# Kernel tuning notes

Measured on AMD Instinct MI355X. Metric: run time of the kernel, lower is better.

Reference implementation:

```python
import jax, jax.numpy as jnp
import numpy as np

L, H, T, C, OUT, B = 8, 16, 2048, 1024, 1024, 4
DH = C // H
EPS = 1e-5


def _sincos_pos_embed(embed_dim, n):
    omega = np.arange(embed_dim // 2, dtype=np.float64) / (embed_dim / 2.0)
    omega = 1.0 / 10000 ** omega
    out = np.einsum('m,d->md', np.arange(n, dtype=np.float64), omega)
    return np.concatenate([np.sin(out), np.cos(out)], axis=1).astype(np.float32)


def setup_inputs() -> dict:
    key = jax.random.key(0)
    ks = jax.random.split(key, 12)
    s = 0.02  # torch init std
    n = lambda k, sh: jax.random.normal(k, sh, jnp.float32) * s
    zc = jnp.zeros((L, C), jnp.float32)
    return {
        'seq': jax.random.normal(ks[0], (B, T, C), jnp.float32),
        'pos_embed': jnp.asarray(_sincos_pos_embed(C, T))[None],  # [1,T,C]
        'Wq': n(ks[1], (L, C, C)), 'bq': zc,
        'Wk': n(ks[2], (L, C, C)), 'bk': zc,
        'Wv': n(ks[3], (L, C, C)), 'bv': zc,
        'Wo': n(ks[4], (L, C, C)), 'bo': zc,
        'ln1_w': jnp.ones((L, C), jnp.float32), 'ln1_b': zc,
        'ln2_w': jnp.ones((L, C), jnp.float32), 'ln2_b': zc,
        'W1': n(ks[5], (L, 4 * C, C)), 'b1': jnp.zeros((L, 4 * C), jnp.float32),
        'W2': n(ks[6], (L, C, 4 * C)), 'b2': zc,
        'lnf_w': jnp.ones((C,), jnp.float32), 'lnf_b': jnp.zeros((C,), jnp.float32),
        'Whead': n(ks[7], (OUT, C)),
    }


def _ln(x, w, b):
    mu = jnp.mean(x, -1, keepdims=True)
    var = jnp.mean(jnp.square(x - mu), -1, keepdims=True)
    return (x - mu) * jax.lax.rsqrt(var + EPS) * w + b


def _block(x, p):
    (Wq, bq, Wk, bk, Wv, bv, Wo, bo, l1w, l1b, l2w, l2b, W1, b1, W2, b2) = p
    b_, t_, c_ = x.shape
    h = _ln(x, l1w, l1b)
    q = (h @ Wq.T + bq).reshape(b_, t_, H, DH)
    k = (h @ Wk.T + bk).reshape(b_, t_, H, DH)
    v = (h @ Wv.T + bv).reshape(b_, t_, H, DH)
    # NOTE: source mask buffer is all ones -> no masking (full softmax)
    att = jnp.einsum('bqhd,bkhd->bhqk', q, k) * (1.0 / np.sqrt(DH))
    att = jax.nn.softmax(att, axis=-1)
    y = jnp.einsum('bhqk,bkhd->bqhd', att, v).reshape(b_, t_, c_)
    x = x + y @ Wo.T + bo
    h2 = _ln(x, l2w, l2b)
    x = x + jax.nn.gelu(h2 @ W1.T + b1, approximate=False) @ W2.T + b2
    return x, None


def reference(seq, pos_embed, Wq, bq, Wk, bk, Wv, bv, Wo, bo,
              ln1_w, ln1_b, ln2_w, ln2_b, W1, b1, W2, b2,
              lnf_w, lnf_b, Whead):
    t = seq.shape[1]
    x = seq + pos_embed[:, -t:, :]  # embedding dropout is identity at eval
    params = (Wq, bq, Wk, bk, Wv, bv, Wo, bo, ln1_w, ln1_b, ln2_w, ln2_b, W1, b1, W2, b2)
    x, _ = jax.lax.scan(_block, x, params)
    x = _ln(x, lnf_w, lnf_b)
    return x @ Whead.T
```

## Files before the change

kernel.cpp:

```cpp
#include <hip/hip_runtime.h>
#include <hip/hip_bf16.h>


#define LAYERS 8
#define NH 16
#define TT 2048
#define CC 1024
#define NB 4
#define MR (NB*TT)
#define LN_EPS 1e-5f

typedef __bf16 bf16_t;
typedef __attribute__((ext_vector_type(8))) __bf16 bf16x8;
typedef __attribute__((ext_vector_type(4))) __bf16 bf16x4;
typedef __attribute__((ext_vector_type(4))) float f32x4;
typedef __attribute__((ext_vector_type(8))) short s16x8;
typedef __attribute__((ext_vector_type(4))) unsigned u32x4;

__device__ inline f32x4 mfma16x16x32(bf16x8 a, bf16x8 b, f32x4 c) {
    return __builtin_amdgcn_mfma_f32_16x16x32_bf16(a, b, c, 0, 0, 0);
}

__device__ inline void gload_lds16(const void* g, void* lds) {
    __builtin_amdgcn_global_load_lds((const __attribute__((address_space(1))) void*)g,
                                     (__attribute__((address_space(3))) void*)lds, 16, 0, 0);
}

__device__ inline unsigned pack_bf16(float a, float b) {
    unsigned short ua = __builtin_bit_cast(unsigned short, (bf16_t)a);
    unsigned short ub = __builtin_bit_cast(unsigned short, (bf16_t)b);
    return (unsigned)ua | ((unsigned)ub << 16);
}


__global__ __launch_bounds__(256) void add_pos_k(const float* __restrict__ s,
                                                 const float* __restrict__ p,
                                                 float* __restrict__ x) {
    int i = blockIdx.x * 256 + threadIdx.x;
    float4 a = ((const float4*)s)[i];
    float4 b = ((const float4*)p)[i & ((TT * CC / 4) - 1)];
    ((float4*)x)[i] = make_float4(a.x + b.x, a.y + b.y, a.z + b.z, a.w + b.w);
}

__global__ __launch_bounds__(256) void f32_to_bf16_k(const float* __restrict__ s,
                                                     bf16_t* __restrict__ d, int n4) {
    int i = blockIdx.x * 256 + threadIdx.x;
    if (i < n4) {
        float4 v = ((const float4*)s)[i];
        bf16x4 o;
        o[0] = (bf16_t)v.x; o[1] = (bf16_t)v.y; o[2] = (bf16_t)v.z; o[3] = (bf16_t)v.w;
        ((bf16x4*)d)[i] = o;
    }
}

__global__ __launch_bounds__(256) void convert_layer_k(
        const float* __restrict__ Wq, const float* __restrict__ Wk,
        const float* __restrict__ Wv, const float* __restrict__ Wo,
        const float* __restrict__ W1, const float* __restrict__ W2,
        const float* __restrict__ bq, const float* __restrict__ bk,
        const float* __restrict__ bv,
        bf16_t* __restrict__ wqkvb, bf16_t* __restrict__ wob,
        bf16_t* __restrict__ w1b, bf16_t* __restrict__ w2b,
        float* __restrict__ bqkv) {
    const int i = blockIdx.x * 256 + threadIdx.x;
    if (i < 3145728) {
        const float4* s4;
        bf16_t* dst;
        int off;
        if (i < 262144)       { s4 = (const float4*)Wq + i;             dst = wqkvb; off = i; }
        else if (i < 524288)  { s4 = (const float4*)Wk + (i - 262144);  dst = wqkvb; off = i; }
        else if (i < 786432)  { s4 = (const float4*)Wv + (i - 524288);  dst = wqkvb; off = i; }
        else if (i < 1048576) { s4 = (const float4*)Wo + (i - 786432);  dst = wob;   off = i - 786432; }
        else if (i < 2097152) { s4 = (const float4*)W1 + (i - 1048576); dst = w1b;   off = i - 1048576; }
        else                  { s4 = (const float4*)W2 + (i - 2097152); dst = w2b;   off = i - 2097152; }
        float4 v = *s4;
        bf16x4 o;
        o[0] = (bf16_t)v.x; o[1] = (bf16_t)v.y; o[2] = (bf16_t)v.z; o[3] = (bf16_t)v.w;
        ((bf16x4*)dst)[off] = o;
    } else if (i < 3146496) {
        const int j = i - 3145728;
        const float* b = (j < 256) ? bq : (j < 512 ? bk : bv);
        ((float4*)bqkv)[j] = ((const float4*)b)[j & 255];
    }
}


__global__ __launch_bounds__(256) void ln_rows_k(const float* __restrict__ x,
                                                 const float* __restrict__ wgt,
                                                 const float* __restrict__ bgt,
                                                 bf16_t* __restrict__ out) {
    const int row = blockIdx.x * 4 + (threadIdx.x >> 6);
    const int l = threadIdx.x & 63;
    const float* xr = x + (size_t)row * CC;
    float4 v[4];
    float s = 0.f, sq = 0.f;
#pragma unroll
    for (int j = 0; j < 4; j++) {
        v[j] = *(const float4*)&xr[j * 256 + l * 4];
        s  += v[j].x + v[j].y + v[j].z + v[j].w;
        sq += v[j].x * v[j].x + v[j].y * v[j].y + v[j].z * v[j].z + v[j].w * v[j].w;
    }
#pragma unroll
    for (int m = 1; m < 64; m <<= 1) { s += __shfl_xor(s, m); sq += __shfl_xor(sq, m); }
    const float mu = s * (1.f / CC);
    const float rstd = rsqrtf(sq * (1.f / CC) - mu * mu + LN_EPS);
#pragma unroll
    for (int j = 0; j < 4; j++) {
        const int c0 = j * 256 + l * 4;
        const float4 wv = *(const float4*)&wgt[c0];
        const float4 bv = *(const float4*)&bgt[c0];
        bf16x4 o;
        o[0] = (bf16_t)((v[j].x - mu) * rstd * wv.x + bv.x);
        o[1] = (bf16_t)((v[j].y - mu) * rstd * wv.y + bv.y);
        o[2] = (bf16_t)((v[j].z - mu) * rstd * wv.z + bv.z);
        o[3] = (bf16_t)((v[j].w - mu) * rstd * wv.w + bv.w);
        *(bf16x4*)&out[(size_t)row * CC + c0] = o;
    }
}


#define EPI_BF16 0
#define EPI_GELU 1
#define EPI_RES  2
#define EPI_F32  3

template <int EPI>
__global__ __launch_bounds__(256) void gemm_bt(const bf16_t* __restrict__ A,
                                               const bf16_t* __restrict__ Bw,
                                               const float* __restrict__ bias,
                                               float* __restrict__ resid,
                                               bf16_t* __restrict__ obf,
                                               float* __restrict__ of32,
                                               int N, int K, int nbn) {
    __shared__ __align__(16) bf16_t As[128 * 32];
    __shared__ __align__(16) bf16_t Bs[128 * 32];
    const int nwg = gridDim.x;
    const int id = blockIdx.x;
    const int swz = (id & 7) * (nwg >> 3) + (id >> 3);
    const int bn = swz % nbn, bm = swz / nbn;
    const int t = threadIdx.x, w = t >> 6, l = t & 63;
    const int wm = (w >> 1) << 6, wn = (w & 1) << 6;
    const int fr = l & 15, fg = l >> 4;
    const int srow = l >> 2, scol = (l & 3) * 8;
    f32x4 acc[4][4] = {};
    for (int k0 = 0; k0 < K; k0 += 32) {
#pragma unroll
        for (int it = 0; it < 2; ++it) {
            const int rr = it * 64 + w * 16;
            gload_lds16(A  + (size_t)(bm * 128 + rr + srow) * K + k0 + scol, &As[rr * 32]);
            gload_lds16(Bw + (size_t)(bn * 128 + rr + srow) * K + k0 + scol, &Bs[rr * 32]);
        }
        __syncthreads();
        bf16x8 af[4], bfv[4];
#pragma unroll
        for (int i = 0; i < 4; i++) af[i]  = *(const bf16x8*)&As[(wm + i * 16 + fr) * 32 + fg * 8];
#pragma unroll
        for (int j = 0; j < 4; j++) bfv[j] = *(const bf16x8*)&Bs[(wn + j * 16 + fr) * 32 + fg * 8];
#pragma unroll
        for (int i = 0; i < 4; i++)
#pragma unroll
            for (int j = 0; j < 4; j++)
                acc[i][j] = mfma16x16x32(af[i], bfv[j], acc[i][j]);
        __syncthreads();
    }
#pragma unroll
    for (int i = 0; i < 4; i++) {
#pragma unroll
        for (int j = 0; j < 4; j++) {
            const int col = bn * 128 + wn + j * 16 + fr;
            float bv = 0.f;
            if constexpr (EPI != EPI_F32) bv = bias[col];
#pragma unroll
            for (int rg = 0; rg < 4; ++rg) {
                const int row = bm * 128 + wm + i * 16 + fg * 4 + rg;
                float v = acc[i][j][rg] + bv;
                if constexpr (EPI == EPI_BF16) {
                    obf[(size_t)row * N + col] = (bf16_t)v;
                } else if constexpr (EPI == EPI_GELU) {
                    v = 0.5f * v * (1.0f + erff(v * 0.70710678118f));
                    obf[(size_t)row * N + col] = (bf16_t)v;
                } else if constexpr (EPI == EPI_RES) {
                    resid[(size_t)row * CC + col] += v;
                } else {
                    of32[(size_t)row * N + col] = v;
                }
            }
        }
    }
}


template <int EPI>
__global__ __launch_bounds__(512, 1) void gemm8p(const bf16_t* __restrict__ A,
                                                 const bf16_t* __restrict__ Bw,
                                                 const float* __restrict__ bias,
                                                 bf16_t* __restrict__ obf,
                                                 int N, int K, int nbn) {
    extern __shared__ __align__(16) char smem[];
    bf16_t* ldsA = (bf16_t*)smem;
    bf16_t* ldsB = (bf16_t*)smem + 24576;
    const int nwg = gridDim.x;
    const int id  = blockIdx.x;
    const int swzid = (id & 7) * (nwg >> 3) + (id >> 3);
    const int bn = swzid % nbn, bm = swzid / nbn;
    const int t = threadIdx.x, wv = t >> 6, lane = t & 63;
    const int fr = lane & 15, fg = lane >> 4;
    const int wm2 = (wv >> 2) * 128, wn2 = (wv & 3) * 64;
    const int swf = ((fr & 8) ? 16 : 0) | ((fr & 4) ? 8 : 0);
    const int rdA0 = (wm2 + fr) * 32 + ((fg * 8) ^ swf);
    const int rdB0 = (wn2 + fr) * 32 + ((fg * 8) ^ swf);
    const int rr0 = wv * 16 + (lane >> 2);
    const int sws = ((rr0 & 8) ? 16 : 0) | ((rr0 & 4) ? 8 : 0);
    const size_t gA0 = (size_t)(bm * 256 + rr0) * K + (((lane & 3) * 8) ^ sws);
    const size_t gB0 = (size_t)(bn * 256 + rr0) * K + (((lane & 3) * 8) ^ sws);
    const int ldsStage = wv * 512;
    const int NT = K >> 5;

    f32x4 acc[8][4] = {};

    auto stA = [&](int T) {
        bf16_t* dst = ldsA + (T % 3) * 8192 + ldsStage;
        const bf16_t* s = A + gA0 + (size_t)T * 32;
        gload_lds16(s, dst);
        gload_lds16(s + (size_t)128 * K, dst + 4096);
    };
    auto stB = [&](int T) {
        bf16_t* dst = ldsB + (T % 3) * 8192 + ldsStage;
        const bf16_t* s = Bw + gB0 + (size_t)T * 32;
        gload_lds16(s, dst);
        gload_lds16(s + (size_t)128 * K, dst + 4096);
    };
    stA(0); stB(0); stA(1); stB(1);

    for (int T = 0; T < NT; ++T) {
        if (T == NT - 1) asm volatile("s_waitcnt vmcnt(0)" ::: "memory");
        else             asm volatile("s_waitcnt vmcnt(4)" ::: "memory");
        __builtin_amdgcn_s_barrier();
        const bf16_t* As_ = ldsA + (T % 3) * 8192;
        const bf16_t* Bs_ = ldsB + (T % 3) * 8192;
        bf16x8 af[4], bf[4];
#pragma unroll
        for (int i = 0; i < 4; i++) af[i] = *(const bf16x8*)&As_[rdA0 + i * 512];
#pragma unroll
        for (int i = 0; i < 4; i++) bf[i] = *(const bf16x8*)&Bs_[rdB0 + i * 512];
        if (T + 2 < NT) stA(T + 2);
        __builtin_amdgcn_s_setprio(1);
#pragma unroll
        for (int mi = 0; mi < 4; mi++)
#pragma unroll
            for (int ni = 0; ni < 4; ni++)
                acc[mi][ni] = mfma16x16x32(af[mi], bf[ni], acc[mi][ni]);
        __builtin_amdgcn_s_setprio(0);
#pragma unroll
        for (int i = 0; i < 4; i++) af[i] = *(const bf16x8*)&As_[rdA0 + (4 + i) * 512];
        if (T + 2 < NT) stB(T + 2);
        __builtin_amdgcn_s_setprio(1);
#pragma unroll
        for (int mi = 0; mi < 4; mi++)
#pragma unroll
            for (int ni = 0; ni < 4; ni++)
                acc[4 + mi][ni] = mfma16x16x32(af[mi], bf[ni], acc[4 + mi][ni]);
        __builtin_amdgcn_s_setprio(0);
    }
#pragma unroll
    for (int mi = 0; mi < 8; mi++) {
#pragma unroll
        for (int ni = 0; ni < 4; ni++) {
            const int col = bn * 256 + wn2 + ni * 16 + fr;
            const float bv = bias[col];
#pragma unroll
            for (int rg = 0; rg < 4; rg++) {
                const int row = bm * 256 + wm2 + mi * 16 + fg * 4 + rg;
                float v = acc[mi][ni][rg] + bv;
                if constexpr (EPI == EPI_GELU)
                    v = 0.5f * v * (1.0f + erff(v * 0.70710678118f));
                obf[(size_t)row * N + col] = (bf16_t)v;
            }
        }
    }
}


__global__ __launch_bounds__(256, 4) void attn_k(const bf16_t* __restrict__ qkv,
                                                 bf16_t* __restrict__ y) {
    __shared__ __align__(16) bf16_t Ks[64 * 64];
    __shared__ __align__(16) bf16_t Vt[64 * 64];
    const int id = blockIdx.x;
    const int swz = (id & 7) * 256 + (id >> 3);
    const int qt = swz & 31, bh = swz >> 5;
    const int b = bh >> 4, h = bh & 15;
    const int t = threadIdx.x, w = t >> 6, l = t & 63;
    const int fr = l & 15, fg = l >> 4;
    const int hh = fg >> 1;
    const int q0 = qt * 64 + w * 16;
    const size_t bT = (size_t)b * TT;
    const float SCL = 0.125f * 1.44269504f;

    bf16x8 qf[2];
    {
        const size_t qoff = (bT + q0 + fr) * 3072 + h * 64 + fg * 8;
        qf[0] = *(const bf16x8*)&qkv[qoff];
        qf[1] = *(const bf16x8*)&qkv[qoff + 32];
    }
    float mrun = -1e30f, lse = 0.f;
    f32x4 oacc[4] = {};

    const int srow = t >> 2;
    const int c8a = (t & 3) * 8;
    const int ksw = (srow & 7) << 4;
    char* KsB = (char*)Ks;
    char* VtB = (char*)Vt;

    s16x8 kr0, kr1, vr0, vr1;
    auto preload = [&](int kv0) {
        const size_t roff = (bT + kv0 + srow) * 3072 + h * 64;
        kr0 = *(const s16x8*)&qkv[roff + 1024 + c8a];
        kr1 = *(const s16x8*)&qkv[roff + 1024 + c8a + 32];
        vr0 = *(const s16x8*)&qkv[roff + 2048 + c8a];
        vr1 = *(const s16x8*)&qkv[roff + 2048 + c8a + 32];
    };
    preload(0);

    for (int kv0 = 0; kv0 < TT; kv0 += 64) {
        __syncthreads();
#pragma unroll
        for (int half = 0; half < 2; ++half) {
            const s16x8 kr = half ? kr1 : kr0;
            const s16x8 vr = half ? vr1 : vr0;
            const int c8 = c8a + half * 32;
            *(s16x8*)(KsB + srow * 128 + ((c8 * 2) ^ ksw)) = kr;
#pragma unroll
            for (int j = 0; j < 8; j++) {
                const int d = c8 + j;
                const int dsw = (((d & 7) ^ ((d >> 3) & 7)) << 4);
                *(short*)(VtB + d * 128 + ((srow * 2) ^ dsw)) = vr[j];
            }
        }
        __syncthreads();
        if (kv0 + 64 < TT) preload(kv0 + 64);

        f32x4 sacc[4] = {};
#pragma unroll
        for (int nt = 0; nt < 4; nt++) {
            const int kr_ = nt * 16 + fr;
            const int sw = (kr_ & 7) << 4;
#pragma unroll
            for (int c = 0; c < 2; c++) {
                bf16x8 kf = *(const bf16x8*)(KsB + kr_ * 128 + ((c * 64 + fg * 16) ^ sw));
                sacc[nt] = mfma16x16x32(kf, qf[c], sacc[nt]);
            }
        }
        float tm = sacc[0][0];
#pragma unroll
        for (int nt = 0; nt < 4; nt++)
#pragma unroll
            for (int rg = 0; rg < 4; rg++) tm = fmaxf(tm, sacc[nt][rg]);
        tm = fmaxf(tm, __shfl_xor(tm, 16));
        tm = fmaxf(tm, __shfl_xor(tm, 32));
        tm *= SCL;
        if (!__all(tm - mrun <= 11.5f)) {
            const float mn = fmaxf(mrun, tm);
            const float co = exp2f(mrun - mn);
            lse *= co; mrun = mn;
            const float cr0 = __shfl(co, fg * 4 + 0);
            const float cr1 = __shfl(co, fg * 4 + 1);
            const float cr2 = __shfl(co, fg * 4 + 2);
            const float cr3 = __shfl(co, fg * 4 + 3);
#pragma unroll
            for (int nd = 0; nd < 4; nd++) {
                oacc[nd][0] *= cr0; oacc[nd][1] *= cr1;
                oacc[nd][2] *= cr2; oacc[nd][3] *= cr3;
            }
        }
        const f32x4 sA0 = hh ? sacc[1] : sacc[0];
        const f32x4 sA1 = hh ? sacc[3] : sacc[2];
        const f32x4 sB0 = hh ? sacc[0] : sacc[1];
        const f32x4 sB1 = hh ? sacc[2] : sacc[3];
        float rs = 0.f;
        unsigned pkA[4], pkB[4];
#pragma unroll
        for (int rg = 0; rg < 4; rg++) {
            const float a0 = exp2f(sA0[rg] * SCL - mrun);
            const float a1 = exp2f(sA1[rg] * SCL - mrun);
            const float b0 = exp2f(sB0[rg] * SCL - mrun);
            const float b1 = exp2f(sB1[rg] * SCL - mrun);
            rs += (a0 + a1) + (b0 + b1);
            pkA[rg] = pack_bf16(a0, a1);
            pkB[rg] = pack_bf16(b0, b1);
        }
        rs += __shfl_xor(rs, 16);
        rs += __shfl_xor(rs, 32);
        lse += rs;
        unsigned s0pk[4], s1pk[4];
#pragma unroll
        for (int rg = 0; rg < 4; rg++) {
            const unsigned r16 = __shfl_xor(pkA[rg], 16);
            const unsigned r32 = __shfl_xor(pkB[rg], 32);
            const unsigned r48 = __shfl_xor(pkB[rg], 48);
            s0pk[rg] = (fg == 0) ? pkA[rg] : (fg == 1) ? r48 : (fg == 2) ? r32 : r16;
            s1pk[rg] = (fg == 0) ? r16 : (fg == 1) ? r32 : (fg == 2) ? r48 : pkA[rg];
        }
        u32x4 w0v, w1v;
        w0v[0] = (s0pk[0] & 0xFFFFu) | (s0pk[1] << 16);
        w0v[1] = (s0pk[2] & 0xFFFFu) | (s0pk[3] << 16);
        w0v[2] = (s1pk[0] & 0xFFFFu) | (s1pk[1] << 16);
        w0v[3] = (s1pk[2] & 0xFFFFu) | (s1pk[3] << 16);
        w1v[0] = (s0pk[0] >> 16) | (s0pk[1] & 0xFFFF0000u);
        w1v[1] = (s0pk[2] >> 16) | (s0pk[3] & 0xFFFF0000u);
        w1v[2] = (s1pk[0] >> 16) | (s1pk[1] & 0xFFFF0000u);
        w1v[3] = (s1pk[2] >> 16) | (s1pk[3] & 0xFFFF0000u);
        const bf16x8 paf0 = __builtin_bit_cast(bf16x8, w0v);
        const bf16x8 paf1 = __builtin_bit_cast(bf16x8, w1v);
#pragma unroll
        for (int nd = 0; nd < 4; nd++) {
            const int dr = nd * 16 + fr;
            const int dsw = (((dr & 7) ^ ((dr >> 3) & 7)) << 4);
            bf16x8 vf0 = *(const bf16x8*)(VtB + dr * 128 + ((fg * 16) ^ dsw));
            oacc[nd] = mfma16x16x32(paf0, vf0, oacc[nd]);
            bf16x8 vf1 = *(const bf16x8*)(VtB + dr * 128 + ((64 + fg * 16) ^ dsw));
            oacc[nd] = mfma16x16x32(paf1, vf1, oacc[nd]);
        }
    }
    const float inv = 1.f / lse;
    const float i0 = __shfl(inv, fg * 4 + 0);
    const float i1 = __shfl(inv, fg * 4 + 1);
    const float i2 = __shfl(inv, fg * 4 + 2);
    const float i3 = __shfl(inv, fg * 4 + 3);
#pragma unroll
    for (int nd = 0; nd < 4; nd++) {
        const size_t ro = (bT + q0 + fg * 4) * CC + h * 64 + nd * 16 + fr;
        y[ro]          = (bf16_t)(oacc[nd][0] * i0);
        y[ro + CC]     = (bf16_t)(oacc[nd][1] * i1);
        y[ro + 2 * CC] = (bf16_t)(oacc[nd][2] * i2);
        y[ro + 3 * CC] = (bf16_t)(oacc[nd][3] * i3);
    }
}


extern "C" void kernel_launch(void* const* d_in, const int* in_sizes, int n_in,
                              void* d_out, int out_size, void* d_ws, size_t ws_size,
                              hipStream_t stream) {
    (void)in_sizes; (void)n_in; (void)out_size; (void)ws_size;
    const float* seq  = (const float*)d_in[0];
    const float* pos  = (const float*)d_in[1];
    const float* Wq   = (const float*)d_in[2];
    const float* bq   = (const float*)d_in[3];
    const float* Wk   = (const float*)d_in[4];
    const float* bk   = (const float*)d_in[5];
    const float* Wv   = (const float*)d_in[6];
    const float* bv   = (const float*)d_in[7];
    const float* Wo   = (const float*)d_in[8];
    const float* bo   = (const float*)d_in[9];
    const float* ln1w = (const float*)d_in[10];
    const float* ln1b = (const float*)d_in[11];
    const float* ln2w = (const float*)d_in[12];
    const float* ln2b = (const float*)d_in[13];
    const float* W1   = (const float*)d_in[14];
    const float* b1   = (const float*)d_in[15];
    const float* W2   = (const float*)d_in[16];
    const float* b2   = (const float*)d_in[17];
    const float* lnfw = (const float*)d_in[18];
    const float* lnfb = (const float*)d_in[19];
    const float* Wh   = (const float*)d_in[20];
    float* out = (float*)d_out;

    char* ws = (char*)d_ws;
    float*  x     = (float*)(ws + 0);
    bf16_t* qkvb  = (bf16_t*)(ws + 33554432);
    bf16_t* yb    = (bf16_t*)(ws + 83886080);
    bf16_t* a1b   = (bf16_t*)(ws + 33554432);
    bf16_t* hb    = (bf16_t*)(ws + 100663296);
    bf16_t* wqkvb = (bf16_t*)(ws + 117440512);
    bf16_t* wob   = (bf16_t*)(ws + 123731968);
    bf16_t* w1b   = (bf16_t*)(ws + 125829120);
    bf16_t* w2b   = (bf16_t*)(ws + 134217728);
    bf16_t* whb   = (bf16_t*)(ws + 142606336);
    float*  bqkv  = (float*)(ws + 144703488);

    hipFuncSetAttribute(reinterpret_cast<const void*>(gemm8p<EPI_BF16>),
                        hipFuncAttributeMaxDynamicSharedMemorySize, 98304);
    hipFuncSetAttribute(reinterpret_cast<const void*>(gemm8p<EPI_GELU>),
                        hipFuncAttributeMaxDynamicSharedMemorySize, 98304);

    f32_to_bf16_k<<<1024, 256, 0, stream>>>(Wh, whb, 262144);
    add_pos_k<<<8192, 256, 0, stream>>>(seq, pos, x);

    for (int l = 0; l < LAYERS; ++l) {
        const size_t wo_ = (size_t)l * CC * CC;
        const size_t w4_ = (size_t)l * 4 * CC * CC;
        convert_layer_k<<<12291, 256, 0, stream>>>(Wq + wo_, Wk + wo_, Wv + wo_, Wo + wo_,
                                                   W1 + w4_, W2 + w4_,
                                                   bq + l * CC, bk + l * CC, bv + l * CC,
                                                   wqkvb, wob, w1b, w2b, bqkv);

        ln_rows_k<<<2048, 256, 0, stream>>>(x, ln1w + l * CC, ln1b + l * CC, hb);
        gemm8p<EPI_BF16><<<384, 512, 98304, stream>>>(hb, wqkvb, bqkv, qkvb,
                                                      3072, 1024, 12);
        attn_k<<<2048, 256, 0, stream>>>(qkvb, yb);
        gemm_bt<EPI_RES><<<512, 256, 0, stream>>>(yb, wob, bo + l * CC, x,
                                                  nullptr, nullptr, 1024, 1024, 8);
        ln_rows_k<<<2048, 256, 0, stream>>>(x, ln2w + l * CC, ln2b + l * CC, hb);
        gemm8p<EPI_GELU><<<512, 512, 98304, stream>>>(hb, w1b, b1 + (size_t)l * 4 * CC,
                                                      a1b, 4096, 1024, 16);
        gemm_bt<EPI_RES><<<512, 256, 0, stream>>>(a1b, w2b, b2 + l * CC, x,
                                                  nullptr, nullptr, 1024, 4096, 8);
    }
    ln_rows_k<<<2048, 256, 0, stream>>>(x, lnfw, lnfb, hb);
    gemm_bt<EPI_F32><<<512, 256, 0, stream>>>(hb, whb, nullptr, nullptr,
                                              nullptr, out, 1024, 1024, 8);
}
```

Baseline: 4.310 ms.

## Process two 16-row query groups per wave in attention to reuse K/V tiles

```diff
diff --git a/kernel.cpp b/kernel.cpp
--- a/kernel.cpp
+++ b/kernel.cpp
@@ -286,24 +286,26 @@
     __shared__ __align__(16) bf16_t Ks[64 * 64];
     __shared__ __align__(16) bf16_t Vt[64 * 64];
     const int id = blockIdx.x;
-    const int swz = (id & 7) * 256 + (id >> 3);
-    const int qt = swz & 31, bh = swz >> 5;
+    const int swz = (id & 7) * 128 + (id >> 3);
+    const int qt = swz & 15, bh = swz >> 4;
     const int b = bh >> 4, h = bh & 15;
     const int t = threadIdx.x, w = t >> 6, l = t & 63;
     const int fr = l & 15, fg = l >> 4;
     const int hh = fg >> 1;
-    const int q0 = qt * 64 + w * 16;
+    const int q0w = qt * 128 + w * 32;
     const size_t bT = (size_t)b * TT;
     const float SCL = 0.125f * 1.44269504f;
 
-    bf16x8 qf[2];
-    {
-        const size_t qoff = (bT + q0 + fr) * 3072 + h * 64 + fg * 8;
-        qf[0] = *(const bf16x8*)&qkv[qoff];
-        qf[1] = *(const bf16x8*)&qkv[qoff + 32];
-    }
-    float mrun = -1e30f, lse = 0.f;
-    f32x4 oacc[4] = {};
+    bf16x8 qf[2][2];
+#pragma unroll
+    for (int g = 0; g < 2; g++) {
+        const size_t qoff = (bT + q0w + g * 16 + fr) * 3072 + h * 64 + fg * 8;
+        qf[g][0] = *(const bf16x8*)&qkv[qoff];
+        qf[g][1] = *(const bf16x8*)&qkv[qoff + 32];
+    }
+    float mrun[2] = {-1e30f, -1e30f};
+    float lse[2] = {0.f, 0.f};
+    f32x4 oacc[2][4] = {};
 
     const int srow = t >> 2;
     const int c8a = (t & 3) * 8;
@@ -339,7 +341,7 @@
         __syncthreads();
         if (kv0 + 64 < TT) preload(kv0 + 64);
 
-        f32x4 sacc[4] = {};
+        f32x4 sacc[2][4] = {};
 #pragma unroll
         for (int nt = 0; nt < 4; nt++) {
             const int kr_ = nt * 16 + fr;
@@ -347,92 +349,102 @@
 #pragma unroll
             for (int c = 0; c < 2; c++) {
                 bf16x8 kf = *(const bf16x8*)(KsB + kr_ * 128 + ((c * 64 + fg * 16) ^ sw));
-                sacc[nt] = mfma16x16x32(kf, qf[c], sacc[nt]);
-            }
-        }
-        float tm = sacc[0][0];
-#pragma unroll
-        for (int nt = 0; nt < 4; nt++)
-#pragma unroll
-            for (int rg = 0; rg < 4; rg++) tm = fmaxf(tm, sacc[nt][rg]);
-        tm = fmaxf(tm, __shfl_xor(tm, 16));
-        tm = fmaxf(tm, __shfl_xor(tm, 32));
-        tm *= SCL;
-        if (!__all(tm - mrun <= 11.5f)) {
-            const float mn = fmaxf(mrun, tm);
-            const float co = exp2f(mrun - mn);
-            lse *= co; mrun = mn;
-            const float cr0 = __shfl(co, fg * 4 + 0);
-            const float cr1 = __shfl(co, fg * 4 + 1);
-            const float cr2 = __shfl(co, fg * 4 + 2);
-            const float cr3 = __shfl(co, fg * 4 + 3);
-#pragma unroll
-            for (int nd = 0; nd < 4; nd++) {
-                oacc[nd][0] *= cr0; oacc[nd][1] *= cr1;
-                oacc[nd][2] *= cr2; oacc[nd][3] *= cr3;
-            }
-        }
-        const f32x4 sA0 = hh ? sacc[1] : sacc[0];
-        const f32x4 sA1 = hh ? sacc[3] : sacc[2];
-        const f32x4 sB0 = hh ? sacc[0] : sacc[1];
-        const f32x4 sB1 = hh ? sacc[2] : sacc[3];
-        float rs = 0.f;
-        unsigned pkA[4], pkB[4];
-#pragma unroll
-        for (int rg = 0; rg < 4; rg++) {
-            const float a0 = exp2f(sA0[rg] * SCL - mrun);
-            const float a1 = exp2f(sA1[rg] * SCL - mrun);
-            const float b0 = exp2f(sB0[rg] * SCL - mrun);
-            const float b1 = exp2f(sB1[rg] * SCL - mrun);
-            rs += (a0 + a1) + (b0 + b1);
-            pkA[rg] = pack_bf16(a0, a1);
-            pkB[rg] = pack_bf16(b0, b1);
-        }
-        rs += __shfl_xor(rs, 16);
-        rs += __shfl_xor(rs, 32);
-        lse += rs;
-        unsigned s0pk[4], s1pk[4];
-#pragma unroll
-        for (int rg = 0; rg < 4; rg++) {
-            const unsigned r16 = __shfl_xor(pkA[rg], 16);
-            const unsigned r32 = __shfl_xor(pkB[rg], 32);
-            const unsigned r48 = __shfl_xor(pkB[rg], 48);
-            s0pk[rg] = (fg == 0) ? pkA[rg] : (fg == 1) ? r48 : (fg == 2) ? r32 : r16;
-            s1pk[rg] = (fg == 0) ? r16 : (fg == 1) ? r32 : (fg == 2) ? r48 : pkA[rg];
-        }
-        u32x4 w0v, w1v;
-        w0v[0] = (s0pk[0] & 0xFFFFu) | (s0pk[1] << 16);
-        w0v[1] = (s0pk[2] & 0xFFFFu) | (s0pk[3] << 16);
-        w0v[2] = (s1pk[0] & 0xFFFFu) | (s1pk[1] << 16);
-        w0v[3] = (s1pk[2] & 0xFFFFu) | (s1pk[3] << 16);
-        w1v[0] = (s0pk[0] >> 16) | (s0pk[1] & 0xFFFF0000u);
-        w1v[1] = (s0pk[2] >> 16) | (s0pk[3] & 0xFFFF0000u);
-        w1v[2] = (s1pk[0] >> 16) | (s1pk[1] & 0xFFFF0000u);
-        w1v[3] = (s1pk[2] >> 16) | (s1pk[3] & 0xFFFF0000u);
-        const bf16x8 paf0 = __builtin_bit_cast(bf16x8, w0v);
-        const bf16x8 paf1 = __builtin_bit_cast(bf16x8, w1v);
+                sacc[0][nt] = mfma16x16x32(kf, qf[0][c], sacc[0][nt]);
+                sacc[1][nt] = mfma16x16x32(kf, qf[1][c], sacc[1][nt]);
+            }
+        }
+        bf16x8 paf[2][2];
+#pragma unroll
+        for (int g = 0; g < 2; g++) {
+            float tm = sacc[g][0][0];
+#pragma unroll
+            for (int nt = 0; nt < 4; nt++)
+#pragma unroll
+                for (int rg = 0; rg < 4; rg++) tm = fmaxf(tm, sacc[g][nt][rg]);
+            tm = fmaxf(tm, __shfl_xor(tm, 16));
+            tm = fmaxf(tm, __shfl_xor(tm, 32));
+            tm *= SCL;
+            if (!__all(tm - mrun[g] <= 11.5f)) {
+                const float mn = fmaxf(mrun[g], tm);
+                const float co = exp2f(mrun[g] - mn);
+                lse[g] *= co; mrun[g] = mn;
+                const float cr0 = __shfl(co, fg * 4 + 0);
+                const float cr1 = __shfl(co, fg * 4 + 1);
+                const float cr2 = __shfl(co, fg * 4 + 2);
+                const float cr3 = __shfl(co, fg * 4 + 3);
+#pragma unroll
+                for (int nd = 0; nd < 4; nd++) {
+                    oacc[g][nd][0] *= cr0; oacc[g][nd][1] *= cr1;
+                    oacc[g][nd][2] *= cr2; oacc[g][nd][3] *= cr3;
+                }
+            }
+            const f32x4 sA0 = hh ? sacc[g][1] : sacc[g][0];
+            const f32x4 sA1 = hh ? sacc[g][3] : sacc[g][2];
+            const f32x4 sB0 = hh ? sacc[g][0] : sacc[g][1];
+            const f32x4 sB1 = hh ? sacc[g][2] : sacc[g][3];
+            float rs = 0.f;
+            unsigned pkA[4], pkB[4];
+#pragma unroll
+            for (int rg = 0; rg < 4; rg++) {
+                const float a0 = exp2f(sA0[rg] * SCL - mrun[g]);
+                const float a1 = exp2f(sA1[rg] * SCL - mrun[g]);
+                const float b0 = exp2f(sB0[rg] * SCL - mrun[g]);
+                const float b1 = exp2f(sB1[rg] * SCL - mrun[g]);
+                rs += (a0 + a1) + (b0 + b1);
+                pkA[rg] = pack_bf16(a0, a1);
+                pkB[rg] = pack_bf16(b0, b1);
+            }
+            rs += __shfl_xor(rs, 16);
+            rs += __shfl_xor(rs, 32);
+            lse[g] += rs;
+            unsigned s0pk[4], s1pk[4];
+#pragma unroll
+            for (int rg = 0; rg < 4; rg++) {
+                const unsigned r16 = __shfl_xor(pkA[rg], 16);
+                const unsigned r32 = __shfl_xor(pkB[rg], 32);
+                const unsigned r48 = __shfl_xor(pkB[rg], 48);
+                s0pk[rg] = (fg == 0) ? pkA[rg] : (fg == 1) ? r48 : (fg == 2) ? r32 : r16;
+                s1pk[rg] = (fg == 0) ? r16 : (fg == 1) ? r32 : (fg == 2) ? r48 : pkA[rg];
+            }
+            u32x4 w0v, w1v;
+            w0v[0] = (s0pk[0] & 0xFFFFu) | (s0pk[1] << 16);
+            w0v[1] = (s0pk[2] & 0xFFFFu) | (s0pk[3] << 16);
+            w0v[2] = (s1pk[0] & 0xFFFFu) | (s1pk[1] << 16);
+            w0v[3] = (s1pk[2] & 0xFFFFu) | (s1pk[3] << 16);
+            w1v[0] = (s0pk[0] >> 16) | (s0pk[1] & 0xFFFF0000u);
+            w1v[1] = (s0pk[2] >> 16) | (s0pk[3] & 0xFFFF0000u);
+            w1v[2] = (s1pk[0] >> 16) | (s1pk[1] & 0xFFFF0000u);
+            w1v[3] = (s1pk[2] >> 16) | (s1pk[3] & 0xFFFF0000u);
+            paf[g][0] = __builtin_bit_cast(bf16x8, w0v);
+            paf[g][1] = __builtin_bit_cast(bf16x8, w1v);
+        }
 #pragma unroll
         for (int nd = 0; nd < 4; nd++) {
             const int dr = nd * 16 + fr;
             const int dsw = (((dr & 7) ^ ((dr >> 3) & 7)) << 4);
             bf16x8 vf0 = *(const bf16x8*)(VtB + dr * 128 + ((fg * 16) ^ dsw));
-            oacc[nd] = mfma16x16x32(paf0, vf0, oacc[nd]);
+            oacc[0][nd] = mfma16x16x32(paf[0][0], vf0, oacc[0][nd]);
+            oacc[1][nd] = mfma16x16x32(paf[1][0], vf0, oacc[1][nd]);
             bf16x8 vf1 = *(const bf16x8*)(VtB + dr * 128 + ((64 + fg * 16) ^ dsw));
-            oacc[nd] = mfma16x16x32(paf1, vf1, oacc[nd]);
-        }
-    }
-    const float inv = 1.f / lse;
-    const float i0 = __shfl(inv, fg * 4 + 0);
-    const float i1 = __shfl(inv, fg * 4 + 1);
-    const float i2 = __shfl(inv, fg * 4 + 2);
-    const float i3 = __shfl(inv, fg * 4 + 3);
-#pragma unroll
-    for (int nd = 0; nd < 4; nd++) {
-        const size_t ro = (bT + q0 + fg * 4) * CC + h * 64 + nd * 16 + fr;
-        y[ro]          = (bf16_t)(oacc[nd][0] * i0);
-        y[ro + CC]     = (bf16_t)(oacc[nd][1] * i1);
-        y[ro + 2 * CC] = (bf16_t)(oacc[nd][2] * i2);
-        y[ro + 3 * CC] = (bf16_t)(oacc[nd][3] * i3);
+            oacc[0][nd] = mfma16x16x32(paf[0][1], vf1, oacc[0][nd]);
+            oacc[1][nd] = mfma16x16x32(paf[1][1], vf1, oacc[1][nd]);
+        }
+    }
+#pragma unroll
+    for (int g = 0; g < 2; g++) {
+        const float inv = 1.f / lse[g];
+        const float i0 = __shfl(inv, fg * 4 + 0);
+        const float i1 = __shfl(inv, fg * 4 + 1);
+        const float i2 = __shfl(inv, fg * 4 + 2);
+        const float i3 = __shfl(inv, fg * 4 + 3);
+#pragma unroll
+        for (int nd = 0; nd < 4; nd++) {
+            const size_t ro = (bT + q0w + g * 16 + fg * 4) * CC + h * 64 + nd * 16 + fr;
+            y[ro]          = (bf16_t)(oacc[g][nd][0] * i0);
+            y[ro + CC]     = (bf16_t)(oacc[g][nd][1] * i1);
+            y[ro + 2 * CC] = (bf16_t)(oacc[g][nd][2] * i2);
+            y[ro + 3 * CC] = (bf16_t)(oacc[g][nd][3] * i3);
+        }
     }
 }
 
@@ -496,7 +508,7 @@
         ln_rows_k<<<2048, 256, 0, stream>>>(x, ln1w + l * CC, ln1b + l * CC, hb);
         gemm8p<EPI_BF16><<<384, 512, 98304, stream>>>(hb, wqkvb, bqkv, qkvb,
                                                       3072, 1024, 12);
-        attn_k<<<2048, 256, 0, stream>>>(qkvb, yb);
+        attn_k<<<1024, 256, 0, stream>>>(qkvb, yb);
         gemm_bt<EPI_RES><<<512, 256, 0, stream>>>(yb, wob, bo + l * CC, x,
                                                   nullptr, nullptr, 1024, 1024, 8);
         ln_rows_k<<<2048, 256, 0, stream>>>(x, ln2w + l * CC, ln2b + l * CC, hb);
```

New measurement: 4.802 ms. +11.4%, slower.
